# Kernel tuning notes

Hardware: AMD Instinct MI355X
Metric: run time of the kernel (lower is better)

## Reference

```python
import jax, jax.numpy as jnp
import numpy as np

NUM_BLOCKS = 16
IN_FEATURES = 4096
OUT_FEATURES = 4096
BLOCK_IN = IN_FEATURES // NUM_BLOCKS
BLOCK_OUT = OUT_FEATURES // NUM_BLOCKS
BATCH = 16384


def setup_inputs() -> dict:
    key = jax.random.key(0)
    kx, kw, kb = jax.random.split(key, 3)
    x = jax.random.normal(kx, (BATCH, IN_FEATURES), dtype=jnp.float32)
    # Per-block weights, matching torch nn.Linear init scale (U[-1/sqrt(in), 1/sqrt(in)])
    bound = 1.0 / np.sqrt(BLOCK_IN)
    W = jax.random.uniform(kw, (NUM_BLOCKS, BLOCK_OUT, BLOCK_IN), minval=-bound, maxval=bound, dtype=jnp.float32)
    b = jax.random.uniform(kb, (NUM_BLOCKS, BLOCK_OUT), minval=-bound, maxval=bound, dtype=jnp.float32)
    return {"x": x, "W": W, "b": b}


def reference(x, W, b):
    # x: [N, in_features] -> [N, nb, block_in]
    n = x.shape[0]
    xb = x.reshape(n, NUM_BLOCKS, BLOCK_IN)
    # per-block linear: y = x @ W_k.T + b_k  (fused block-diagonal GEMM)
    yb = jnp.einsum('nki,koi->nko', xb, W) + b  # [N, nb, block_out]
    return yb.reshape(n, OUT_FEATURES)
```

## Files before the change

### kernel.cpp

```cpp
#include <hip/hip_runtime.h>

typedef short short8 __attribute__((ext_vector_type(8)));
typedef float floatx4 __attribute__((ext_vector_type(4)));
typedef int intx4 __attribute__((ext_vector_type(4)));

#define INF 4096
#define TROWS 32
#define RSTRIDE 1040
#define TBYTES (TROWS * RSTRIDE)

__device__ __forceinline__ ushort f2bf(float f) {
  unsigned u = __builtin_bit_cast(unsigned, f);
  u += 0x7fffu + ((u >> 16) & 1u);
  return (ushort)(u >> 16);
}

__global__ __launch_bounds__(512, 1) void bd_gemm(
    const float* __restrict__ x, const float* __restrict__ W,
    const float* __restrict__ bias, float* __restrict__ out)
{
  __shared__ __align__(16) char xlds[4 * TBYTES];

  const int bid  = blockIdx.x;
  const int kb   = bid & 15;
  const int mg   = bid >> 4;
  const int tid  = threadIdx.x;
  const int lane = tid & 63;
  const int w    = tid >> 6;
  const int ln   = lane & 15;
  const int lk   = lane >> 4;

  const float* xbase = x   + (size_t)(mg * 1024) * INF + kb * 256;
  float*       obase = out + (size_t)(mg * 1024) * INF + kb * 256 + w * 32;

#define WAITVM(N) asm volatile("s_waitcnt vmcnt(" #N ")" ::: "memory")
#define BAR()                                                                 \
  do {                                                                        \
    asm volatile("" ::: "memory");                                            \
    __builtin_amdgcn_s_barrier();                                             \
    asm volatile("" ::: "memory");                                            \
  } while (0)

#define PREFETCH(t)                                                           \
  _Pragma("unroll") for (int i_ = 0; i_ < 4; ++i_) {                          \
    const int r_ = w * 4 + i_;                                                \
    const float* gp_ = xbase + (size_t)((t) * TROWS + r_) * INF + lane * 4;   \
    __builtin_amdgcn_global_load_lds(                                         \
        (const __attribute__((address_space(1))) float*)gp_,                  \
        (__attribute__((address_space(3))) float*)(                           \
            xlds + ((t) & 3) * TBYTES + r_ * RSTRIDE),                        \
        16, 0, 0);                                                            \
  }

#define COMPUTE(t, accv)                                                      \
  {                                                                           \
    const char* bb_ = xlds + ((t) & 3) * TBYTES;                              \
    _Pragma("unroll") for (int a_ = 0; a_ < 4; ++a_)                          \
      _Pragma("unroll") for (int e_ = 0; e_ < 4; ++e_) accv[a_][e_] = 0.0f;   \
    _Pragma("unroll") for (int kc_ = 0; kc_ < 8; ++kc_) {                     \
      short8 xf_[2];                                                          \
      _Pragma("unroll") for (int mi_ = 0; mi_ < 2; ++mi_) {                   \
        const char* fp_ = bb_ + (mi_ * 16 + ln) * RSTRIDE + kc_ * 128 + lk * 32; \
        floatx4 v0_ = *(const floatx4*)fp_;                                   \
        floatx4 v1_ = *(const floatx4*)(fp_ + 16);                            \
        unsigned p0_, p1_, p2_, p3_;                                          \
        asm("v_cvt_pk_bf16_f32 %0, %1, %2" : "=v"(p0_) : "v"(v0_[0]), "v"(v0_[1])); \
        asm("v_cvt_pk_bf16_f32 %0, %1, %2" : "=v"(p1_) : "v"(v0_[2]), "v"(v0_[3])); \
        asm("v_cvt_pk_bf16_f32 %0, %1, %2" : "=v"(p2_) : "v"(v1_[0]), "v"(v1_[1])); \
        asm("v_cvt_pk_bf16_f32 %0, %1, %2" : "=v"(p3_) : "v"(v1_[2]), "v"(v1_[3])); \
        intx4 d_;                                                             \
        d_[0] = (int)p0_; d_[1] = (int)p1_; d_[2] = (int)p2_; d_[3] = (int)p3_; \
        xf_[mi_] = __builtin_bit_cast(short8, d_);                            \
      }                                                                       \
      _Pragma("unroll") for (int mi_ = 0; mi_ < 2; ++mi_)                     \
        _Pragma("unroll") for (int ni_ = 0; ni_ < 2; ++ni_)                   \
          accv[mi_ * 2 + ni_] = __builtin_amdgcn_mfma_f32_16x16x32_bf16(      \
              wf[ni_][kc_], xf_[mi_], accv[mi_ * 2 + ni_], 0, 0, 0);          \
    }                                                                         \
  }

#define STOREACC(t, accv)                                                     \
  _Pragma("unroll") for (int mi_ = 0; mi_ < 2; ++mi_)                         \
    _Pragma("unroll") for (int ni_ = 0; ni_ < 2; ++ni_) {                     \
      floatx4 r_ = accv[mi_ * 2 + ni_];                                       \
      _Pragma("unroll") for (int j_ = 0; j_ < 4; ++j_) r_[j_] += bv[ni_][j_]; \
      *(floatx4*)(obase + (size_t)((t) * TROWS + mi_ * 16 + ln) * INF +       \
                  ni_ * 16 + lk * 4) = r_;                                    \
    }

  PREFETCH(0)
  PREFETCH(1)
  PREFETCH(2)

  short8 wf[2][8];
  {
    const float* wp = W + (size_t)kb * 65536 + (w * 32 + ln) * 256 + lk * 8;
#pragma unroll
    for (int ni = 0; ni < 2; ++ni)
#pragma unroll
      for (int kc = 0; kc < 8; ++kc) {
        const float* s = wp + ni * 16 * 256 + kc * 32;
        floatx4 v0 = *(const floatx4*)s;
        floatx4 v1 = *(const floatx4*)(s + 4);
        short8 u;
#pragma unroll
        for (int j = 0; j < 4; ++j) {
          u[j]     = (short)f2bf(v0[j]);
          u[4 + j] = (short)f2bf(v1[j]);
        }
        wf[ni][kc] = u;
      }
  }
  floatx4 bv[2];
#pragma unroll
  for (int ni = 0; ni < 2; ++ni)
    bv[ni] = *(const floatx4*)(bias + kb * 256 + w * 32 + ni * 16 + lk * 4);

  floatx4 acc0[4], acc1[4];

  WAITVM(8); BAR(); PREFETCH(3); COMPUTE(0, acc0);

#pragma unroll 1
  for (int tt = 0; tt < 14; ++tt) {
    const int t_ = 1 + tt * 2;
    WAITVM(8); BAR(); PREFETCH(t_ + 3); STOREACC(t_ - 1, acc0); COMPUTE(t_, acc1);
    WAITVM(8); BAR(); PREFETCH(t_ + 4); STOREACC(t_,     acc1); COMPUTE(t_ + 1, acc0);
  }
  WAITVM(8); BAR(); STOREACC(28, acc0); COMPUTE(29, acc1);
  WAITVM(4); BAR(); STOREACC(29, acc1); COMPUTE(30, acc0);
  WAITVM(0); BAR(); STOREACC(30, acc0); COMPUTE(31, acc1);
  STOREACC(31, acc1);

#undef WAITVM
#undef BAR
#undef PREFETCH
#undef COMPUTE
#undef STOREACC
}

extern "C" void kernel_launch(void* const* d_in, const int* in_sizes, int n_in,
                              void* d_out, int out_size, void* d_ws, size_t ws_size,
                              hipStream_t stream) {
  const float* x = (const float*)d_in[0];
  const float* W = (const float*)d_in[1];
  const float* b = (const float*)d_in[2];
  float* out = (float*)d_out;
  hipLaunchKernelGGL(bd_gemm, dim3(256), dim3(512), 0, stream, x, W, b, out);
}
```

Measured before the change: 114.1 us.

## Convert x to bf16 before LDS staging with register double-buffering

```diff
diff --git a/kernel.cpp b/kernel.cpp
--- a/kernel.cpp
+++ b/kernel.cpp
@@ -2,12 +2,12 @@
 
 typedef short short8 __attribute__((ext_vector_type(8)));
 typedef float floatx4 __attribute__((ext_vector_type(4)));
-typedef int intx4 __attribute__((ext_vector_type(4)));
+typedef unsigned uint2v __attribute__((ext_vector_type(2)));
 
 #define INF 4096
 #define TROWS 32
-#define RSTRIDE 1040
-#define TBYTES (TROWS * RSTRIDE)
+#define RS 528
+#define TB (TROWS * RS)
 
 __device__ __forceinline__ ushort f2bf(float f) {
   unsigned u = __builtin_bit_cast(unsigned, f);
@@ -19,7 +19,7 @@
     const float* __restrict__ x, const float* __restrict__ W,
     const float* __restrict__ bias, float* __restrict__ out)
 {
-  __shared__ __align__(16) char xlds[4 * TBYTES];
+  __shared__ __align__(16) char xlds[2 * TB];
 
   const int bid  = blockIdx.x;
   const int kb   = bid & 15;
@@ -33,64 +33,55 @@
   const float* xbase = x   + (size_t)(mg * 1024) * INF + kb * 256;
   float*       obase = out + (size_t)(mg * 1024) * INF + kb * 256 + w * 32;
 
-#define WAITVM(N) asm volatile("s_waitcnt vmcnt(" #N ")" ::: "memory")
-#define BAR()                                                                 \
+#define LGKM0_BAR()                                                           \
   do {                                                                        \
-    asm volatile("" ::: "memory");                                            \
+    asm volatile("s_waitcnt lgkmcnt(0)" ::: "memory");                        \
     __builtin_amdgcn_s_barrier();                                             \
     asm volatile("" ::: "memory");                                            \
   } while (0)
 
-#define PREFETCH(t)                                                           \
+  floatx4 g[4];
+
+#define LOADX(t)                                                              \
+  _Pragma("unroll") for (int i_ = 0; i_ < 4; ++i_)                            \
+    g[i_] = *(const floatx4*)(xbase + (size_t)((t) * TROWS + w * 4 + i_) * INF + lane * 4);
+
+#define WRITEX(t)                                                             \
   _Pragma("unroll") for (int i_ = 0; i_ < 4; ++i_) {                          \
     const int r_ = w * 4 + i_;                                                \
-    const float* gp_ = xbase + (size_t)((t) * TROWS + r_) * INF + lane * 4;   \
-    __builtin_amdgcn_global_load_lds(                                         \
-        (const __attribute__((address_space(1))) float*)gp_,                  \
-        (__attribute__((address_space(3))) float*)(                           \
-            xlds + ((t) & 3) * TBYTES + r_ * RSTRIDE),                        \
-        16, 0, 0);                                                            \
+    unsigned p0_, p1_;                                                        \
+    asm("v_cvt_pk_bf16_f32 %0, %1, %2" : "=v"(p0_) : "v"(g[i_][0]), "v"(g[i_][1])); \
+    asm("v_cvt_pk_bf16_f32 %0, %1, %2" : "=v"(p1_) : "v"(g[i_][2]), "v"(g[i_][3])); \
+    uint2v u_; u_[0] = p0_; u_[1] = p1_;                                      \
+    *(uint2v*)(xlds + ((t) & 1) * TB + r_ * RS + lane * 8) = u_;              \
   }
 
-#define COMPUTE(t, accv)                                                      \
+#define COMPUTE(t)                                                            \
   {                                                                           \
-    const char* bb_ = xlds + ((t) & 3) * TBYTES;                              \
+    const char* bb_ = xlds + ((t) & 1) * TB;                                  \
     _Pragma("unroll") for (int a_ = 0; a_ < 4; ++a_)                          \
-      _Pragma("unroll") for (int e_ = 0; e_ < 4; ++e_) accv[a_][e_] = 0.0f;   \
+      _Pragma("unroll") for (int e_ = 0; e_ < 4; ++e_) acc[a_][e_] = 0.0f;    \
     _Pragma("unroll") for (int kc_ = 0; kc_ < 8; ++kc_) {                     \
       short8 xf_[2];                                                          \
-      _Pragma("unroll") for (int mi_ = 0; mi_ < 2; ++mi_) {                   \
-        const char* fp_ = bb_ + (mi_ * 16 + ln) * RSTRIDE + kc_ * 128 + lk * 32; \
-        floatx4 v0_ = *(const floatx4*)fp_;                                   \
-        floatx4 v1_ = *(const floatx4*)(fp_ + 16);                            \
-        unsigned p0_, p1_, p2_, p3_;                                          \
-        asm("v_cvt_pk_bf16_f32 %0, %1, %2" : "=v"(p0_) : "v"(v0_[0]), "v"(v0_[1])); \
-        asm("v_cvt_pk_bf16_f32 %0, %1, %2" : "=v"(p1_) : "v"(v0_[2]), "v"(v0_[3])); \
-        asm("v_cvt_pk_bf16_f32 %0, %1, %2" : "=v"(p2_) : "v"(v1_[0]), "v"(v1_[1])); \
-        asm("v_cvt_pk_bf16_f32 %0, %1, %2" : "=v"(p3_) : "v"(v1_[2]), "v"(v1_[3])); \
-        intx4 d_;                                                             \
-        d_[0] = (int)p0_; d_[1] = (int)p1_; d_[2] = (int)p2_; d_[3] = (int)p3_; \
-        xf_[mi_] = __builtin_bit_cast(short8, d_);                            \
-      }                                                                       \
+      _Pragma("unroll") for (int mi_ = 0; mi_ < 2; ++mi_)                     \
+        xf_[mi_] = *(const short8*)(bb_ + (mi_ * 16 + ln) * RS + kc_ * 64 + lk * 16); \
       _Pragma("unroll") for (int mi_ = 0; mi_ < 2; ++mi_)                     \
         _Pragma("unroll") for (int ni_ = 0; ni_ < 2; ++ni_)                   \
-          accv[mi_ * 2 + ni_] = __builtin_amdgcn_mfma_f32_16x16x32_bf16(      \
-              wf[ni_][kc_], xf_[mi_], accv[mi_ * 2 + ni_], 0, 0, 0);          \
+          acc[mi_ * 2 + ni_] = __builtin_amdgcn_mfma_f32_16x16x32_bf16(       \
+              wf[ni_][kc_], xf_[mi_], acc[mi_ * 2 + ni_], 0, 0, 0);           \
     }                                                                         \
   }
 
-#define STOREACC(t, accv)                                                     \
+#define STOREACC(t)                                                           \
   _Pragma("unroll") for (int mi_ = 0; mi_ < 2; ++mi_)                         \
     _Pragma("unroll") for (int ni_ = 0; ni_ < 2; ++ni_) {                     \
-      floatx4 r_ = accv[mi_ * 2 + ni_];                                       \
+      floatx4 r_ = acc[mi_ * 2 + ni_];                                        \
       _Pragma("unroll") for (int j_ = 0; j_ < 4; ++j_) r_[j_] += bv[ni_][j_]; \
       *(floatx4*)(obase + (size_t)((t) * TROWS + mi_ * 16 + ln) * INF +       \
                   ni_ * 16 + lk * 4) = r_;                                    \
     }
 
-  PREFETCH(0)
-  PREFETCH(1)
-  PREFETCH(2)
+  LOADX(0)
 
   short8 wf[2][8];
   {
@@ -116,24 +107,25 @@
   for (int ni = 0; ni < 2; ++ni)
     bv[ni] = *(const floatx4*)(bias + kb * 256 + w * 32 + ni * 16 + lk * 4);
 
-  floatx4 acc0[4], acc1[4];
+  floatx4 acc[4];
 
-  WAITVM(8); BAR(); PREFETCH(3); COMPUTE(0, acc0);
+  WRITEX(0)
+  LGKM0_BAR();
 
 #pragma unroll 1
-  for (int tt = 0; tt < 14; ++tt) {
-    const int t_ = 1 + tt * 2;
-    WAITVM(8); BAR(); PREFETCH(t_ + 3); STOREACC(t_ - 1, acc0); COMPUTE(t_, acc1);
-    WAITVM(8); BAR(); PREFETCH(t_ + 4); STOREACC(t_,     acc1); COMPUTE(t_ + 1, acc0);
+  for (int t = 0; t < 32; ++t) {
+    if (t < 31) LOADX(t + 1)
+    COMPUTE(t)
+    STOREACC(t)
+    if (t < 31) {
+      WRITEX(t + 1)
+      LGKM0_BAR();
+    }
   }
-  WAITVM(8); BAR(); STOREACC(28, acc0); COMPUTE(29, acc1);
-  WAITVM(4); BAR(); STOREACC(29, acc1); COMPUTE(30, acc0);
-  WAITVM(0); BAR(); STOREACC(30, acc0); COMPUTE(31, acc1);
-  STOREACC(31, acc1);
 
-#undef WAITVM
-#undef BAR
-#undef PREFETCH
+#undef LGKM0_BAR
+#undef LOADX
+#undef WRITEX
 #undef COMPUTE
 #undef STOREACC
 }
```

New measurement: 108.5 us. 4.8% less time.
